# Performance work log

Measured on AMD Instinct MI355X. Metric: run time of the kernel, lower is better.

The kernel has to match this reference:

```python
import jax, jax.numpy as jnp
import numpy as np

B, D_IN, UNITS = 4096, 1024, 1024


def setup_inputs() -> dict:
    key = jax.random.key(0)
    ks = jax.random.split(key, 8)
    scale = 1.0 / np.sqrt(D_IN + UNITS)
    return {
        "inputs": jax.random.normal(ks[0], (B, D_IN), jnp.float32),
        "hidden_state": jax.random.normal(ks[1], (B, UNITS), jnp.float32),
        "cell_state": jax.random.normal(ks[2], (B, UNITS), jnp.float32),
        "W_f": jax.random.normal(ks[3], (D_IN + UNITS, UNITS), jnp.float32) * scale,
        "b_f": jnp.ones((UNITS,), jnp.float32),  # forget gate bias initialized to ones
        "W_i": jax.random.normal(ks[4], (D_IN + UNITS, UNITS), jnp.float32) * scale,
        "b_i": jnp.zeros((UNITS,), jnp.float32),
        "W_c": jax.random.normal(ks[5], (D_IN + UNITS, UNITS), jnp.float32) * scale,
        "b_c": jnp.zeros((UNITS,), jnp.float32),
        "W_o": jax.random.normal(ks[6], (D_IN + UNITS, UNITS), jnp.float32) * scale,
        "b_o": jnp.zeros((UNITS,), jnp.float32),
    }


def reference(inputs, hidden_state, cell_state, W_f, b_f, W_i, b_i, W_c, b_c, W_o, b_o):
    # concat (hidden, inputs) along feature axis -> [B, UNITS + D_IN]
    x = jnp.concatenate((hidden_state, inputs), axis=1)
    # fuse the 4 gate projections into one GEMM: [B, 4*UNITS]
    W = jnp.concatenate((W_f, W_i, W_c, W_o), axis=1)
    b = jnp.concatenate((b_f, b_i, b_c, b_o), axis=0)
    gates = x @ W + b
    f, i, c, o = jnp.split(gates, 4, axis=1)
    forget_gate = jax.nn.sigmoid(f)
    input_gate = jax.nn.sigmoid(i)
    state_candidates = jnp.tanh(c)
    output_gate = jax.nn.sigmoid(o)
    new_cell = forget_gate * cell_state + input_gate * state_candidates
    new_hidden = output_gate * jnp.tanh(new_cell)
    return (new_hidden, new_cell)
```

## Files before the change

### kernel.cpp

```cpp
#include <hip/hip_runtime.h>

#define MDIM 4096
#define KDIM 2048
#define UDIM 1024
#define CMOFF (MDIM * UDIM)
#define NK 64
#define THREADS 512

typedef __bf16 bfrag __attribute__((ext_vector_type(8)));
typedef float f32x4 __attribute__((ext_vector_type(4)));

#define GLDS(gsrc, ldst)                                                                  \
  __builtin_amdgcn_global_load_lds((const __attribute__((address_space(1))) void*)(gsrc), \
                                   (__attribute__((address_space(3))) void*)(ldst), 16, 0, 0)

__device__ __forceinline__ unsigned short f2bf(float x) {
  unsigned int u = __float_as_uint(x);
  unsigned int r = (u + 0x7fffu + ((u >> 16) & 1u)) >> 16;
  return (unsigned short)r;
}

__device__ __forceinline__ float fast_sigmoid(float x) { return 1.f / (1.f + __expf(-x)); }

__device__ __forceinline__ float fast_tanh(float x) {
  float ax = fabsf(x);
  float e = __expf(-2.f * ax);
  float r = (1.f - e) / (1.f + e);
  return copysignf(r, x);
}

__global__ void pack_x(const float* __restrict__ hidden, const float* __restrict__ inputs,
                       unsigned short* __restrict__ A) {
  int t = blockIdx.x * blockDim.x + threadIdx.x;
  int e = t * 4;
  int m = e >> 11;
  int c = e & 2047;
  const float* src = (c < 1024) ? (hidden + m * 1024 + c) : (inputs + m * 1024 + (c - 1024));
  float4 v = *(const float4*)src;
  ushort4 o;
  o.x = f2bf(v.x);
  o.y = f2bf(v.y);
  o.z = f2bf(v.z);
  o.w = f2bf(v.w);
  *(ushort4*)(A + e) = o;
}

__global__ void pack_w(const float* __restrict__ Wf, const float* __restrict__ Wi,
                       const float* __restrict__ Wc, const float* __restrict__ Wo,
                       unsigned short* __restrict__ Wt) {
  __shared__ float tile[32][33];
  const int k0 = blockIdx.x * 32;
  const int u0 = blockIdx.y * 32;
  const int g = blockIdx.z;
  const float* W = (g == 0) ? Wf : (g == 1) ? Wi : (g == 2) ? Wc : Wo;
  const int t = threadIdx.x;
  {
    int kk = t >> 3, uu = (t & 7) * 4;
    float4 v = *(const float4*)(W + (k0 + kk) * UDIM + u0 + uu);
    tile[kk][uu + 0] = v.x;
    tile[kk][uu + 1] = v.y;
    tile[kk][uu + 2] = v.z;
    tile[kk][uu + 3] = v.w;
  }
  __syncthreads();
  {
    int ur = t >> 3, k4 = (t & 7) * 4;
    ushort4 o;
    o.x = f2bf(tile[k4 + 0][ur]);
    o.y = f2bf(tile[k4 + 1][ur]);
    o.z = f2bf(tile[k4 + 2][ur]);
    o.w = f2bf(tile[k4 + 3][ur]);
    *(ushort4*)(Wt + (size_t)(g * UDIM + u0 + ur) * KDIM + k0 + k4) = o;
  }
}

__global__ __launch_bounds__(THREADS, 2) void lstm_gemm(
    const unsigned short* __restrict__ A, const unsigned short* __restrict__ Wt,
    const float* __restrict__ bf_, const float* __restrict__ bi_,
    const float* __restrict__ bc_, const float* __restrict__ bo_,
    const float* __restrict__ cell, float* __restrict__ out) {
  extern __shared__ __bf16 lds[];

  const int tid = threadIdx.x;
  const int lane = tid & 63;
  const int wid = tid >> 6;
  const int wr = wid >> 2;
  const int wc = wid & 3;
  const int lrow = lane & 15;
  const int gb = lane >> 4;

  const int wg = blockIdx.x;
  const int swz = (wg & 7) * 32 + (wg >> 3);
  const int m0 = (swz >> 4) * 256;
  const int bn = swz & 15;

  const int G0 = tid, G1 = THREADS + tid;
  const int ar0 = G0 >> 2, ar1 = G1 >> 2;
  const unsigned short* aS0 =
      A + (size_t)(m0 + ar0) * KDIM + (((G0 & 3) ^ ((ar0 >> 1) & 3)) * 8);
  const unsigned short* aS1 =
      A + (size_t)(m0 + ar1) * KDIM + (((G1 & 3) ^ ((ar1 >> 1) & 3)) * 8);
  const int nr0 = G0 >> 2, nr1 = G1 >> 2;
  const int u_0 = bn * 64 + ((nr0 >> 6) << 4) + (nr0 & 15);
  const int u_1 = bn * 64 + ((nr1 >> 6) << 4) + (nr1 & 15);
  const int g_0 = (nr0 >> 4) & 3;
  const int g_1 = (nr1 >> 4) & 3;
  const unsigned short* bS0 =
      Wt + (size_t)(g_0 * UDIM + u_0) * KDIM + (((G0 & 3) ^ ((nr0 >> 1) & 3)) * 8);
  const unsigned short* bS1 =
      Wt + (size_t)(g_1 * UDIM + u_1) * KDIM + (((G1 & 3) ^ ((nr1 >> 1) & 3)) * 8);

  int aoff[8];
#pragma unroll
  for (int mi = 0; mi < 8; ++mi) {
    const int R = wr * 128 + mi * 16 + lrow;
    aoff[mi] = R * 32 + ((gb ^ ((R >> 1) & 3)) * 8);
  }
  int boff[4];
#pragma unroll
  for (int nf = 0; nf < 4; ++nf) {
    const int n = wc * 64 + nf * 16 + lrow;
    boff[nf] = 8192 + n * 32 + ((gb ^ ((n >> 1) & 3)) * 8);
  }

  f32x4 acc[8][4];
#pragma unroll
  for (int mi = 0; mi < 8; ++mi)
#pragma unroll
    for (int nf = 0; nf < 4; ++nf) acc[mi][nf] = (f32x4){0.f, 0.f, 0.f, 0.f};

#define STAGE_A(T, SR)                        \
  do {                                        \
    __bf16* dst_ = lds + (SR) * 16384;        \
    GLDS(aS0 + (T) * 32, dst_ + G0 * 8);      \
    GLDS(aS1 + (T) * 32, dst_ + G1 * 8);      \
  } while (0)
#define STAGE_B(T, SR)                        \
  do {                                        \
    __bf16* dst_ = lds + (SR) * 16384 + 8192; \
    GLDS(bS0 + (T) * 32, dst_ + G0 * 8);      \
    GLDS(bS1 + (T) * 32, dst_ + G1 * 8);      \
  } while (0)

#define VM8 asm volatile("s_waitcnt vmcnt(8)" ::: "memory")
#define VM4 asm volatile("s_waitcnt vmcnt(4)" ::: "memory")
#define VM0 asm volatile("s_waitcnt vmcnt(0)" ::: "memory")

  STAGE_A(0, 0);
  STAGE_B(0, 0);
  STAGE_A(1, 1);
  STAGE_B(1, 1);
  STAGE_A(2, 2);
  STAGE_B(2, 2);

#define TILE_BODY(T, R, SR, DO_STAGE, WAITCODE)                                            \
  do {                                                                                     \
    WAITCODE;                                                                              \
    __builtin_amdgcn_s_barrier();                                                          \
    __bf16* ldsr_ = lds + (R) * 16384;                                                     \
    bfrag Am[4], Bm[4];                                                                    \
    _Pragma("unroll") for (int mi = 0; mi < 4; ++mi) Am[mi] =                              \
        *(const bfrag*)(ldsr_ + aoff[mi]);                                                 \
    _Pragma("unroll") for (int nf = 0; nf < 4; ++nf) Bm[nf] =                              \
        *(const bfrag*)(ldsr_ + boff[nf]);                                                 \
    if (DO_STAGE) STAGE_A((T) + 3, SR);                                                    \
    __builtin_amdgcn_s_setprio(1);                                                         \
    _Pragma("unroll") for (int mi = 0; mi < 4; ++mi)                                       \
        _Pragma("unroll") for (int nf = 0; nf < 4; ++nf) acc[mi][nf] =                     \
            __builtin_amdgcn_mfma_f32_16x16x32_bf16(Am[mi], Bm[nf], acc[mi][nf], 0, 0, 0); \
    __builtin_amdgcn_s_setprio(0);                                                         \
    bfrag A2[4];                                                                           \
    _Pragma("unroll") for (int mi = 0; mi < 4; ++mi) A2[mi] =                              \
        *(const bfrag*)(ldsr_ + aoff[4 + mi]);                                             \
    if (DO_STAGE) STAGE_B((T) + 3, SR);                                                    \
    __builtin_amdgcn_s_setprio(1);                                                         \
    _Pragma("unroll") for (int mi = 0; mi < 4; ++mi)                                       \
        _Pragma("unroll") for (int nf = 0; nf < 4; ++nf) acc[4 + mi][nf] =                 \
            __builtin_amdgcn_mfma_f32_16x16x32_bf16(A2[mi], Bm[nf], acc[4 + mi][nf], 0, 0, 0); \
    __builtin_amdgcn_s_setprio(0);                                                         \
  } while (0)

  for (int t = 0; t < NK - 4; t += 4) {
    TILE_BODY(t + 0, 0, 3, 1, VM8);
    TILE_BODY(t + 1, 1, 0, 1, VM8);
    TILE_BODY(t + 2, 2, 1, 1, VM8);
    TILE_BODY(t + 3, 3, 2, 1, VM8);
  }
  TILE_BODY(NK - 4, 0, 3, 1, VM8);
  TILE_BODY(NK - 3, 1, 0, 0, VM8);
  TILE_BODY(NK - 2, 2, 0, 0, VM4);
  TILE_BODY(NK - 1, 3, 0, 0, VM0);

  const int u = bn * 64 + wc * 16 + lrow;
  const float fb = bf_[u], ib = bi_[u], cb = bc_[u], ob = bo_[u];
  const int rbase = m0 + wr * 128 + (lane >> 4) * 4;
#pragma unroll
  for (int mi = 0; mi < 8; ++mi) {
#pragma unroll
    for (int j = 0; j < 4; ++j) {
      const int m = rbase + mi * 16 + j;
      float pf = acc[mi][0][j] + fb;
      float pi = acc[mi][1][j] + ib;
      float pc = acc[mi][2][j] + cb;
      float po = acc[mi][3][j] + ob;
      float fg = fast_sigmoid(pf);
      float ig = fast_sigmoid(pi);
      float cc = fast_tanh(pc);
      float og = fast_sigmoid(po);
      float cold = cell[(size_t)m * UDIM + u];
      float cnew = fg * cold + ig * cc;
      out[(size_t)m * UDIM + u] = og * fast_tanh(cnew);
      out[CMOFF + (size_t)m * UDIM + u] = cnew;
    }
  }
}

extern "C" void kernel_launch(void* const* d_in, const int* in_sizes, int n_in,
                              void* d_out, int out_size, void* d_ws, size_t ws_size,
                              hipStream_t stream) {
  const float* inputs = (const float*)d_in[0];
  const float* hidden = (const float*)d_in[1];
  const float* cell = (const float*)d_in[2];
  const float* Wf = (const float*)d_in[3];
  const float* bf = (const float*)d_in[4];
  const float* Wi = (const float*)d_in[5];
  const float* bi = (const float*)d_in[6];
  const float* Wc = (const float*)d_in[7];
  const float* bc = (const float*)d_in[8];
  const float* Wo = (const float*)d_in[9];
  const float* bo = (const float*)d_in[10];
  float* out = (float*)d_out;

  unsigned short* Abf = (unsigned short*)d_ws;
  unsigned short* Wt = Abf + (size_t)MDIM * KDIM;

  pack_x<<<(MDIM * KDIM / 4) / 256, 256, 0, stream>>>(hidden, inputs, Abf);
  pack_w<<<dim3(KDIM / 32, UDIM / 32, 4), 256, 0, stream>>>(Wf, Wi, Wc, Wo, Wt);
  lstm_gemm<<<dim3(256), dim3(THREADS), 131072, stream>>>(Abf, Wt, bf, bi, bc, bo, cell, out);
}
```

Before: 89.88 us.

## Restructure GEMM main loop into 64-wide K steps with 4-phase ping-pong pipeline

Replaces the 4-stage, 32-wide-K LDS ring with a 2-buffer, 64-wide-K scheme split into half-tiles. Each K step runs four barrier-separated phases that interleave LDS fragment loads, global-to-LDS staging of the next tile and MFMA clusters. It also switches to an 8-way XOR swizzle for the wider rows. The goal is better overlap of loads with MFMA work and fewer LDS bank conflicts. In exchange it adds more barriers per K step and a shallower prefetch depth, which can stall if memory latency is not hidden.

```diff
diff --git a/kernel.cpp b/kernel.cpp
--- a/kernel.cpp
+++ b/kernel.cpp
@@ -4,7 +4,6 @@
 #define KDIM 2048
 #define UDIM 1024
 #define CMOFF (MDIM * UDIM)
-#define NK 64
 #define THREADS 512
 
 typedef __bf16 bfrag __attribute__((ext_vector_type(8)));
@@ -88,40 +87,42 @@
   const int wc = wid & 3;
   const int lrow = lane & 15;
   const int gb = lane >> 4;
+  const int l7 = lrow & 7;
 
   const int wg = blockIdx.x;
   const int swz = (wg & 7) * 32 + (wg >> 3);
   const int m0 = (swz >> 4) * 256;
   const int bn = swz & 15;
 
-  const int G0 = tid, G1 = THREADS + tid;
-  const int ar0 = G0 >> 2, ar1 = G1 >> 2;
-  const unsigned short* aS0 =
-      A + (size_t)(m0 + ar0) * KDIM + (((G0 & 3) ^ ((ar0 >> 1) & 3)) * 8);
-  const unsigned short* aS1 =
-      A + (size_t)(m0 + ar1) * KDIM + (((G1 & 3) ^ ((ar1 >> 1) & 3)) * 8);
-  const int nr0 = G0 >> 2, nr1 = G1 >> 2;
-  const int u_0 = bn * 64 + ((nr0 >> 6) << 4) + (nr0 & 15);
-  const int u_1 = bn * 64 + ((nr1 >> 6) << 4) + (nr1 & 15);
-  const int g_0 = (nr0 >> 4) & 3;
-  const int g_1 = (nr1 >> 4) & 3;
-  const unsigned short* bS0 =
-      Wt + (size_t)(g_0 * UDIM + u_0) * KDIM + (((G0 & 3) ^ ((nr0 >> 1) & 3)) * 8);
-  const unsigned short* bS1 =
-      Wt + (size_t)(g_1 * UDIM + u_1) * KDIM + (((G1 & 3) ^ ((nr1 >> 1) & 3)) * 8);
-
-  int aoff[8];
-#pragma unroll
-  for (int mi = 0; mi < 8; ++mi) {
-    const int R = wr * 128 + mi * 16 + lrow;
-    aoff[mi] = R * 32 + ((gb ^ ((R >> 1) & 3)) * 8);
-  }
-  int boff[4];
-#pragma unroll
-  for (int nf = 0; nf < 4; ++nf) {
-    const int n = wc * 64 + nf * 16 + lrow;
-    boff[nf] = 8192 + n * 32 + ((gb ^ ((n >> 1) & 3)) * 8);
-  }
+  const int t8 = tid >> 3;
+  const int gsrc = (tid & 7) ^ (t8 & 7);
+  const unsigned short* aS00 = A + (size_t)(m0 + t8) * KDIM + gsrc * 8;
+  const unsigned short* aS01 = A + (size_t)(m0 + 128 + t8) * KDIM + gsrc * 8;
+  const unsigned short* aS10 = A + (size_t)(m0 + 64 + t8) * KDIM + gsrc * 8;
+  const unsigned short* aS11 = A + (size_t)(m0 + 192 + t8) * KDIM + gsrc * 8;
+  int br00, br01, br10, br11;
+  {
+    int rp0 = t8, rp1 = 64 + t8;
+    br00 = (0 * 2 + ((rp0 >> 4) & 1)) * 1024 + bn * 64 + (rp0 >> 5) * 16 + (rp0 & 15);
+    br01 = (0 * 2 + ((rp1 >> 4) & 1)) * 1024 + bn * 64 + (rp1 >> 5) * 16 + (rp1 & 15);
+    br10 = (1 * 2 + ((rp0 >> 4) & 1)) * 1024 + bn * 64 + (rp0 >> 5) * 16 + (rp0 & 15);
+    br11 = (1 * 2 + ((rp1 >> 4) & 1)) * 1024 + bn * 64 + (rp1 >> 5) * 16 + (rp1 & 15);
+  }
+  const unsigned short* bS00 = Wt + (size_t)br00 * KDIM + gsrc * 8;
+  const unsigned short* bS01 = Wt + (size_t)br01 * KDIM + gsrc * 8;
+  const unsigned short* bS10 = Wt + (size_t)br10 * KDIM + gsrc * 8;
+  const unsigned short* bS11 = Wt + (size_t)br11 * KDIM + gsrc * 8;
+
+  const int sw0 = (gb ^ l7) * 8;
+  const int sw1 = ((4 + gb) ^ l7) * 8;
+  const __bf16* pA00 = lds + (wr * 64 + lrow) * 64 + sw0;
+  const __bf16* pA01 = lds + (wr * 64 + lrow) * 64 + sw1;
+  const __bf16* pB00 = lds + 16384 + (wc * 32 + lrow) * 64 + sw0;
+  const __bf16* pB01 = lds + 16384 + (wc * 32 + lrow) * 64 + sw1;
+  const __bf16* pA10 = pA00 + 32768;
+  const __bf16* pA11 = pA01 + 32768;
+  const __bf16* pB10 = pB00 + 32768;
+  const __bf16* pB11 = pB01 + 32768;
 
   f32x4 acc[8][4];
 #pragma unroll
@@ -129,67 +130,94 @@
 #pragma unroll
     for (int nf = 0; nf < 4; ++nf) acc[mi][nf] = (f32x4){0.f, 0.f, 0.f, 0.f};
 
-#define STAGE_A(T, SR)                        \
-  do {                                        \
-    __bf16* dst_ = lds + (SR) * 16384;        \
-    GLDS(aS0 + (T) * 32, dst_ + G0 * 8);      \
-    GLDS(aS1 + (T) * 32, dst_ + G1 * 8);      \
-  } while (0)
-#define STAGE_B(T, SR)                        \
-  do {                                        \
-    __bf16* dst_ = lds + (SR) * 16384 + 8192; \
-    GLDS(bS0 + (T) * 32, dst_ + G0 * 8);      \
-    GLDS(bS1 + (T) * 32, dst_ + G1 * 8);      \
-  } while (0)
-
-#define VM8 asm volatile("s_waitcnt vmcnt(8)" ::: "memory")
+  bfrag Af[4][2], Ag[4][2], Bf01[2][2], Bf23[2][2];
+
+#define STG_A(ND, H, SS)                                                      \
+  do {                                                                        \
+    GLDS(aS##H##0 + (SS) * 64, lds + (ND) + (H) * 8192 + tid * 8);            \
+    GLDS(aS##H##1 + (SS) * 64, lds + (ND) + (H) * 8192 + 4096 + tid * 8);     \
+  } while (0)
+#define STG_B(ND, H, SS)                                                          \
+  do {                                                                            \
+    GLDS(bS##H##0 + (SS) * 64, lds + (ND) + 16384 + (H) * 8192 + tid * 8);        \
+    GLDS(bS##H##1 + (SS) * 64, lds + (ND) + 16384 + (H) * 8192 + 4096 + tid * 8); \
+  } while (0)
+
 #define VM4 asm volatile("s_waitcnt vmcnt(4)" ::: "memory")
+#define VM2 asm volatile("s_waitcnt vmcnt(2)" ::: "memory")
 #define VM0 asm volatile("s_waitcnt vmcnt(0)" ::: "memory")
 
-  STAGE_A(0, 0);
-  STAGE_B(0, 0);
-  STAGE_A(1, 1);
-  STAGE_B(1, 1);
-  STAGE_A(2, 2);
-  STAGE_B(2, 2);
-
-#define TILE_BODY(T, R, SR, DO_STAGE, WAITCODE)                                            \
-  do {                                                                                     \
-    WAITCODE;                                                                              \
-    __builtin_amdgcn_s_barrier();                                                          \
-    __bf16* ldsr_ = lds + (R) * 16384;                                                     \
-    bfrag Am[4], Bm[4];                                                                    \
-    _Pragma("unroll") for (int mi = 0; mi < 4; ++mi) Am[mi] =                              \
-        *(const bfrag*)(ldsr_ + aoff[mi]);                                                 \
-    _Pragma("unroll") for (int nf = 0; nf < 4; ++nf) Bm[nf] =                              \
-        *(const bfrag*)(ldsr_ + boff[nf]);                                                 \
-    if (DO_STAGE) STAGE_A((T) + 3, SR);                                                    \
-    __builtin_amdgcn_s_setprio(1);                                                         \
-    _Pragma("unroll") for (int mi = 0; mi < 4; ++mi)                                       \
-        _Pragma("unroll") for (int nf = 0; nf < 4; ++nf) acc[mi][nf] =                     \
-            __builtin_amdgcn_mfma_f32_16x16x32_bf16(Am[mi], Bm[nf], acc[mi][nf], 0, 0, 0); \
-    __builtin_amdgcn_s_setprio(0);                                                         \
-    bfrag A2[4];                                                                           \
-    _Pragma("unroll") for (int mi = 0; mi < 4; ++mi) A2[mi] =                              \
-        *(const bfrag*)(ldsr_ + aoff[4 + mi]);                                             \
-    if (DO_STAGE) STAGE_B((T) + 3, SR);                                                    \
-    __builtin_amdgcn_s_setprio(1);                                                         \
-    _Pragma("unroll") for (int mi = 0; mi < 4; ++mi)                                       \
-        _Pragma("unroll") for (int nf = 0; nf < 4; ++nf) acc[4 + mi][nf] =                 \
-            __builtin_amdgcn_mfma_f32_16x16x32_bf16(A2[mi], Bm[nf], acc[4 + mi][nf], 0, 0, 0); \
-    __builtin_amdgcn_s_setprio(0);                                                         \
-  } while (0)
-
-  for (int t = 0; t < NK - 4; t += 4) {
-    TILE_BODY(t + 0, 0, 3, 1, VM8);
-    TILE_BODY(t + 1, 1, 0, 1, VM8);
-    TILE_BODY(t + 2, 2, 1, 1, VM8);
-    TILE_BODY(t + 3, 3, 2, 1, VM8);
-  }
-  TILE_BODY(NK - 4, 0, 3, 1, VM8);
-  TILE_BODY(NK - 3, 1, 0, 0, VM8);
-  TILE_BODY(NK - 2, 2, 0, 0, VM4);
-  TILE_BODY(NK - 1, 3, 0, 0, VM0);
+#define PH(CLUSTER, WAIT)                                \
+  do {                                                   \
+    __builtin_amdgcn_sched_barrier(0);                   \
+    __builtin_amdgcn_s_barrier();                        \
+    asm volatile("s_waitcnt lgkmcnt(0)" ::: "memory");   \
+    __builtin_amdgcn_sched_barrier(0);                   \
+    __builtin_amdgcn_s_setprio(1);                       \
+    CLUSTER;                                             \
+    __builtin_amdgcn_s_setprio(0);                       \
+    WAIT;                                                \
+    __builtin_amdgcn_s_barrier();                        \
+  } while (0)
+
+#define CL8(MB, AF, N0, N1, BF)                                                       \
+  _Pragma("unroll") for (int kk = 0; kk < 2; ++kk)                                    \
+      _Pragma("unroll") for (int mi = 0; mi < 4; ++mi) {                              \
+    acc[(MB) + mi][N0] = __builtin_amdgcn_mfma_f32_16x16x32_bf16(                     \
+        AF[mi][kk], BF[0][kk], acc[(MB) + mi][N0], 0, 0, 0);                          \
+    acc[(MB) + mi][N1] = __builtin_amdgcn_mfma_f32_16x16x32_bf16(                     \
+        AF[mi][kk], BF[1][kk], acc[(MB) + mi][N1], 0, 0, 0);                          \
+  }
+
+#define KSTEP(PA0, PA1, PB0, PB1, ND, SS, STG, W1, W2, W4)          \
+  do {                                                              \
+                  \
+    _Pragma("unroll") for (int mi = 0; mi < 4; ++mi) {              \
+      Af[mi][0] = *(const bfrag*)((PA0) + mi * 1024);               \
+      Af[mi][1] = *(const bfrag*)((PA1) + mi * 1024);               \
+    }                                                               \
+    _Pragma("unroll") for (int nf = 0; nf < 2; ++nf) {              \
+      Bf01[nf][0] = *(const bfrag*)((PB0) + nf * 1024);             \
+      Bf01[nf][1] = *(const bfrag*)((PB1) + nf * 1024);             \
+    }                                                               \
+    if (STG) STG_A(ND, 0, SS);                                      \
+    PH(CL8(0, Af, 0, 1, Bf01), W1);                                 \
+                                   \
+    _Pragma("unroll") for (int nf = 0; nf < 2; ++nf) {              \
+      Bf23[nf][0] = *(const bfrag*)((PB0) + 8192 + nf * 1024);      \
+      Bf23[nf][1] = *(const bfrag*)((PB1) + 8192 + nf * 1024);      \
+    }                                                               \
+    if (STG) STG_B(ND, 0, SS);                                      \
+    PH(CL8(0, Af, 2, 3, Bf23), W2);                                 \
+                                   \
+    _Pragma("unroll") for (int mi = 0; mi < 4; ++mi) {              \
+      Ag[mi][0] = *(const bfrag*)((PA0) + 8192 + mi * 1024);        \
+      Ag[mi][1] = *(const bfrag*)((PA1) + 8192 + mi * 1024);        \
+    }                                                               \
+    if (STG) STG_B(ND, 1, SS);                                      \
+    PH(CL8(4, Ag, 2, 3, Bf23), ((void)0));                          \
+                           \
+    _Pragma("unroll") for (int nf = 0; nf < 2; ++nf) {              \
+      Bf01[nf][0] = *(const bfrag*)((PB0) + nf * 1024);             \
+      Bf01[nf][1] = *(const bfrag*)((PB1) + nf * 1024);             \
+    }                                                               \
+    if (STG) STG_A(ND, 1, SS);                                      \
+    PH(CL8(4, Ag, 0, 1, Bf01), W4);                                 \
+  } while (0)
+
+  STG_A(0, 0, 0);
+  STG_B(0, 0, 0);
+  STG_B(0, 1, 0);
+  STG_A(0, 1, 0);
+  VM4;
+  __builtin_amdgcn_s_barrier();
+
+  for (int su = 0; su < 15; ++su) {
+    KSTEP(pA00, pA01, pB00, pB01, 32768, 2 * su + 1, 1, VM4, VM4, VM4);
+    KSTEP(pA10, pA11, pB10, pB11, 0, 2 * su + 2, 1, VM4, VM4, VM4);
+  }
+  KSTEP(pA00, pA01, pB00, pB01, 32768, 31, 1, VM4, VM4, VM4);
+  KSTEP(pA10, pA11, pB10, pB11, 0, 0, 0, VM2, VM0, ((void)0));
 
   const int u = bn * 64 + wc * 16 + lrow;
   const float fb = bf_[u], ib = bi_[u], cb = bc_[u], ob = bo_[u];
```

Measured after the change: 91.56 us. Within noise of the previous version (+1.9%).
